# Kernel optimization log

Measured on AMD Instinct MI355X. Metric: run time of the kernel, lower is better.

The kernel has to match this reference:

```python
import jax, jax.numpy as jnp
import numpy as np

N = 200_000      # n_reflns
NIMG = 500       # n_images
DMETA = 24       # metadata features
WIDTH = 32       # mlp_width
HID = 64         # hidden_units = 2*width (FeedForward default)
DEPTH = 20       # mlp_depth
NPOST = 2        # Normal posterior: (loc, scale)
EPS = 1e-12
KLW = 0.01       # scaling_kl_weight


def setup_inputs() -> dict:
    key = jax.random.key(0)
    ks = jax.random.split(key, 10)
    metadata = jax.random.normal(ks[0], (N, DMETA), jnp.float32)
    iobs = jax.random.normal(ks[1], (N, 1), jnp.float32)
    sigiobs = jax.random.uniform(ks[2], (N, 1), jnp.float32)
    image_ids = jnp.sort(jax.random.randint(ks[3], (N,), 0, NIMG)).astype(jnp.int32)
    n_reflns_per_image = jnp.bincount(image_ids, length=NIMG).astype(jnp.int32)
    d_img = DMETA + 2  # concat(metadata, iobs, sigiobs)
    w_img_in = jax.random.normal(ks[4], (d_img, WIDTH), jnp.float32) / np.float32(np.sqrt(d_img))
    b_img_in = jnp.zeros((WIDTH,), jnp.float32)
    w_scale_in = jax.random.normal(ks[5], (DMETA, WIDTH), jnp.float32) / np.float32(np.sqrt(DMETA))
    b_scale_in = jnp.zeros((WIDTH,), jnp.float32)
    # shared residual FeedForward stack (share_weights=True): x + W2 @ relu(W1 @ x)
    mlp_w1 = jax.random.normal(ks[6], (DEPTH, WIDTH, HID), jnp.float32) / np.float32(np.sqrt(WIDTH))
    mlp_b1 = jnp.zeros((DEPTH, HID), jnp.float32)
    mlp_w2 = jax.random.normal(ks[7], (DEPTH, HID, WIDTH), jnp.float32) * np.float32(0.1 / np.sqrt(HID))
    mlp_b2 = jnp.zeros((DEPTH, WIDTH), jnp.float32)
    w_out = jax.random.normal(ks[8], (WIDTH, NPOST), jnp.float32) / np.float32(np.sqrt(WIDTH))
    b_out = jnp.zeros((NPOST,), jnp.float32)
    return {
        'metadata': metadata, 'iobs': iobs, 'sigiobs': sigiobs,
        'w_img_in': w_img_in, 'b_img_in': b_img_in,
        'w_scale_in': w_scale_in, 'b_scale_in': b_scale_in,
        'mlp_w1': mlp_w1, 'mlp_b1': mlp_b1, 'mlp_w2': mlp_w2, 'mlp_b2': mlp_b2,
        'w_out': w_out, 'b_out': b_out,
        'image_ids_in_this_batch': image_ids,
        'n_reflns_per_image': n_reflns_per_image,
        'mc_samples': 32,
    }


def _mlp(h, w1, b1, w2, b2):
    # depth residual FF blocks, weights stacked along leading DEPTH axis
    def block(h, ws):
        wa, ba, wb, bb = ws
        h = h + (jax.nn.relu(h @ wa + ba) @ wb + bb)
        return h, None
    h, _ = jax.lax.scan(block, h, (w1, b1, w2, b2))
    return h


def reference(metadata, iobs, sigiobs,
              w_img_in, b_img_in, w_scale_in, b_scale_in,
              mlp_w1, mlp_b1, mlp_w2, mlp_b2, w_out, b_out,
              image_ids_in_this_batch, n_reflns_per_image, mc_samples):
    image = jnp.concatenate([metadata, iobs, sigiobs], axis=-1)   # (N, DMETA+2)
    h = image @ w_img_in + b_img_in                               # (N, W)
    h = _mlp(h, mlp_w1, mlp_b1, mlp_w2, mlp_b2)
    nimg = n_reflns_per_image.shape[0]
    sums = jax.ops.segment_sum(h, image_ids_in_this_batch, num_segments=nimg)
    counts = jnp.maximum(n_reflns_per_image, 1).astype(h.dtype)[:, None]
    pooled = sums / counts                                        # (NIMG, W) image-average pool
    s = metadata @ w_scale_in + b_scale_in + pooled[image_ids_in_this_batch]
    s = _mlp(s, mlp_w1, mlp_b1, mlp_w2, mlp_b2)                   # shared weights
    params = s @ w_out + b_out                                    # (N, 2)
    loc = params[:, 0]
    scale = jax.nn.softplus(params[:, 1]) + EPS
    # rsample from Normal(loc, scale), mc_samples draws
    noise = jax.random.normal(jax.random.key(42), (mc_samples, loc.shape[0]), loc.dtype)
    z = loc + scale * noise                                       # (S, N)
    # MC KL estimate: mean_s[log q(z) - log p(z)], p = Laplace(0, 1)
    log_q = -0.5 * jnp.square(noise) - jnp.log(scale) - np.float32(0.5 * np.log(2.0 * np.pi))
    log_p = -jnp.abs(z) - np.float32(np.log(2.0))
    kl_div = KLW * jnp.mean(log_q - log_p, axis=0)                # (N,)
    return z.T, kl_div
```

## Files before the change

### kernel.cpp

```cpp
#include <hip/hip_runtime.h>
#include <stdint.h>

#define N_ROWS 200000
#define NIMG   500
#define DMETA  24
#define WIDTH  32
#define HID    64
#define DEPTH  20
#define MC     32


#define WB      64000
#define LSTR2   16768
#define OFF_WI  (WB + DEPTH * LSTR2)
#define OFF_WS  (OFF_WI + 4096)
#define OFF_BIQ (OFF_WS + 4096)
#define OFF_BSQ (OFF_BIQ + 128)
#define OFF_WOQ (OFF_BSQ + 128)

typedef __attribute__((ext_vector_type(8))) short bf16x8;
typedef __attribute__((ext_vector_type(4))) float f32x4;
typedef __attribute__((ext_vector_type(16))) float f32x16;

#define MFMA32(a, b, acc) __builtin_amdgcn_mfma_f32_32x32x16_bf16((a), (b), (acc), 0, 0, 0)
#define SWP(x, y) asm("v_permlane32_swap_b32 %0, %1" : "+v"(x), "+v"(y))
#define WOFFi(h5, reg) ((((reg) & 3) + 8 * ((reg) >> 2)) + 4 * (h5))

__device__ __forceinline__ uint32_t rotl32(uint32_t x, int r) {
    return (x << r) | (x >> (32 - r));
}

__device__ __forceinline__ uint32_t tf_bits(uint32_t j) {
    const uint32_t ks1 = 42u, ks2 = 0x1BD11BDAu ^ 42u;
    uint32_t x0 = 0u, x1 = j + ks1;
#define R4(a,b,c,d) \
    x0 += x1; x1 = rotl32(x1,(a)); x1 ^= x0; \
    x0 += x1; x1 = rotl32(x1,(b)); x1 ^= x0; \
    x0 += x1; x1 = rotl32(x1,(c)); x1 ^= x0; \
    x0 += x1; x1 = rotl32(x1,(d)); x1 ^= x0;
    R4(13,15,26,6)  x0 += ks1; x1 += ks2 + 1u;
    R4(17,29,16,24) x0 += ks2; x1 += 0u + 2u;
    R4(13,15,26,6)                x1 += ks1 + 3u;
    R4(17,29,16,24) x0 += ks1; x1 += ks2 + 4u;
    R4(13,15,26,6)  x0 += ks2; x1 += 0u + 5u;
#undef R4
    return x0 ^ x1;
}

__device__ __forceinline__ float bits_to_normal(uint32_t b) {
    float f = __uint_as_float((b >> 9) | 0x3f800000u) - 1.0f;
    const float lo = -0.99999994f;
    float u = fmaxf(lo, f * 2.0f + lo);
    return 1.41421356f * erfinvf(u);
}

__device__ __forceinline__ void split1(float x, short& hi, short& lo) {
    uint32_t b = __float_as_uint(x);
    uint32_t a = b + 0x8000u;
    hi = (short)(a >> 16);
    float r = x - __uint_as_float(a & 0xFFFF0000u);
    lo = (short)(__float_as_uint(r) >> 16);
}

__device__ __forceinline__ void split8p(const float* x, bf16x8& hi, bf16x8& lo) {
    uint32_t hu[4], lu[4];
#pragma unroll
    for (int p = 0; p < 4; ++p) {
        float x0 = x[2 * p], x1 = x[2 * p + 1];
        uint32_t h;
        asm("v_cvt_pk_bf16_f32 %0, %1, %2" : "=v"(h) : "v"(x0), "v"(x1));
        float r0 = x0 - __uint_as_float(h << 16);
        float r1 = x1 - __uint_as_float(h & 0xFFFF0000u);
        uint32_t l;
        asm("v_cvt_pk_bf16_f32 %0, %1, %2" : "=v"(l) : "v"(r0), "v"(r1));
        hu[p] = h;
        lu[p] = l;
    }
    __builtin_memcpy(&hi, hu, 16);
    __builtin_memcpy(&lo, lu, 16);
}

__device__ __forceinline__ void mkbfrag(const float* h, bf16x8* Bh, bf16x8* Bl) {
    uint32_t Hh[8], Hl[8];
#pragma unroll
    for (int p = 0; p < 8; ++p) {
        float x0 = h[2 * p], x1 = h[2 * p + 1];
        uint32_t wd;
        asm("v_cvt_pk_bf16_f32 %0, %1, %2" : "=v"(wd) : "v"(x0), "v"(x1));
        float r0 = x0 - __uint_as_float(wd << 16);
        float r1 = x1 - __uint_as_float(wd & 0xFFFF0000u);
        uint32_t ld;
        asm("v_cvt_pk_bf16_f32 %0, %1, %2" : "=v"(ld) : "v"(r0), "v"(r1));
        Hh[p] = wd;
        Hl[p] = ld;
    }
    SWP(Hh[0], Hh[2]); SWP(Hh[1], Hh[3]); SWP(Hh[4], Hh[6]); SWP(Hh[5], Hh[7]);
    SWP(Hl[0], Hl[2]); SWP(Hl[1], Hl[3]); SWP(Hl[4], Hl[6]); SWP(Hl[5], Hl[7]);
    __builtin_memcpy(&Bh[0], &Hh[0], 16);
    __builtin_memcpy(&Bh[1], &Hh[4], 16);
    __builtin_memcpy(&Bl[0], &Hl[0], 16);
    __builtin_memcpy(&Bl[1], &Hl[4], 16);
}

__device__ __forceinline__ void mlp20_x2(float* h0, float* h1,
                                         const char* __restrict__ wsb,
                                         int lane, int h5) {
    uint32_t lb = WB;
    const uint32_t lf = (uint32_t)(lane * 16);
#pragma unroll 1
    for (int l = 0; l < DEPTH; ++l) {
        bf16x8 B0h[2], B0l[2], B1h[2], B1l[2];
        mkbfrag(h0, B0h, B0l);
        mkbfrag(h1, B1h, B1l);
        uint32_t P0[16], P1[16];
#pragma unroll
        for (int tm = 0; tm < 2; ++tm) {
            f32x16 acc0, acc1;
            {
                const char* bq = wsb + lb + 16384u + (uint32_t)(tm * 128 + h5 * 64);
#pragma unroll
                for (int r = 0; r < 4; ++r) {
                    f32x4 q = *(const f32x4*)(bq + 16 * r);
#pragma unroll
                    for (int i = 0; i < 4; ++i) {
                        acc0[4 * r + i] = q[i];
                        acc1[4 * r + i] = q[i];
                    }
                }
            }
            const char* fa = wsb + lb + lf + (uint32_t)(tm * 4096);
            bf16x8 a0h = *(const bf16x8*)(fa);
            bf16x8 a0l = *(const bf16x8*)(fa + 1024);
            bf16x8 a1h = *(const bf16x8*)(fa + 2048);
            bf16x8 a1l = *(const bf16x8*)(fa + 3072);
            acc0 = MFMA32(a0h, B0h[0], acc0);
            acc1 = MFMA32(a0h, B1h[0], acc1);
            acc0 = MFMA32(a0h, B0l[0], acc0);
            acc1 = MFMA32(a0h, B1l[0], acc1);
            acc0 = MFMA32(a0l, B0h[0], acc0);
            acc1 = MFMA32(a0l, B1h[0], acc1);
            acc0 = MFMA32(a1h, B0h[1], acc0);
            acc1 = MFMA32(a1h, B1h[1], acc1);
            acc0 = MFMA32(a1h, B0l[1], acc0);
            acc1 = MFMA32(a1h, B1l[1], acc1);
            acc0 = MFMA32(a1l, B0h[1], acc0);
            acc1 = MFMA32(a1l, B1h[1], acc1);
#pragma unroll
            for (int p = 0; p < 8; ++p) {
                float f0 = fmaxf(acc0[2 * p], 0.0f);
                float f1 = fmaxf(acc0[2 * p + 1], 0.0f);
                uint32_t wd;
                asm("v_cvt_pk_bf16_f32 %0, %1, %2" : "=v"(wd) : "v"(f0), "v"(f1));
                P0[tm * 8 + p] = wd;
                float g0 = fmaxf(acc1[2 * p], 0.0f);
                float g1 = fmaxf(acc1[2 * p + 1], 0.0f);
                uint32_t we;
                asm("v_cvt_pk_bf16_f32 %0, %1, %2" : "=v"(we) : "v"(g0), "v"(g1));
                P1[tm * 8 + p] = we;
            }
        }
        SWP(P0[0], P0[2]);  SWP(P0[1], P0[3]);  SWP(P0[4], P0[6]);   SWP(P0[5], P0[7]);
        SWP(P0[8], P0[10]); SWP(P0[9], P0[11]); SWP(P0[12], P0[14]); SWP(P0[13], P0[15]);
        SWP(P1[0], P1[2]);  SWP(P1[1], P1[3]);  SWP(P1[4], P1[6]);   SWP(P1[5], P1[7]);
        SWP(P1[8], P1[10]); SWP(P1[9], P1[11]); SWP(P1[12], P1[14]); SWP(P1[13], P1[15]);
        f32x16 acc20, acc21;
        {
            const char* bq = wsb + lb + 16640u + (uint32_t)(h5 * 64);
#pragma unroll
            for (int r = 0; r < 4; ++r) {
                f32x4 q = *(const f32x4*)(bq + 16 * r);
#pragma unroll
                for (int i = 0; i < 4; ++i) {
                    acc20[4 * r + i] = h0[4 * r + i] + q[i];
                    acc21[4 * r + i] = h1[4 * r + i] + q[i];
                }
            }
        }
#pragma unroll
        for (int ks = 0; ks < 4; ++ks) {
            bf16x8 Bk0, Bk1;
            __builtin_memcpy(&Bk0, &P0[ks * 4], 16);
            __builtin_memcpy(&Bk1, &P1[ks * 4], 16);
            const char* fa = wsb + lb + lf + 8192u + (uint32_t)(ks * 2048);
            bf16x8 ah = *(const bf16x8*)(fa);
            bf16x8 al = *(const bf16x8*)(fa + 1024);
            acc20 = MFMA32(ah, Bk0, acc20);
            acc21 = MFMA32(ah, Bk1, acc21);
            acc20 = MFMA32(al, Bk0, acc20);
            acc21 = MFMA32(al, Bk1, acc21);
        }
#pragma unroll
        for (int i = 0; i < 16; ++i) { h0[i] = acc20[i]; h1[i] = acc21[i]; }
        lb += LSTR2;
    }
}

__device__ __forceinline__ void input_proj32_x2(
    const bf16x8* X0, const bf16x8* X1,
    const char* __restrict__ wsb, uint32_t wfoff, uint32_t bqoff,
    float* h0, float* h1, int lane, int h5) {
    f32x16 acc0, acc1;
    {
        const char* bq = wsb + bqoff + (uint32_t)(h5 * 64);
#pragma unroll
        for (int r = 0; r < 4; ++r) {
            f32x4 q = *(const f32x4*)(bq + 16 * r);
#pragma unroll
            for (int i = 0; i < 4; ++i) { acc0[4 * r + i] = q[i]; acc1[4 * r + i] = q[i]; }
        }
    }
    const char* fa = wsb + wfoff + (uint32_t)(lane * 16);
    bf16x8 a0h = *(const bf16x8*)(fa);
    bf16x8 a0l = *(const bf16x8*)(fa + 1024);
    bf16x8 a1h = *(const bf16x8*)(fa + 2048);
    bf16x8 a1l = *(const bf16x8*)(fa + 3072);
    acc0 = MFMA32(a0h, X0[0], acc0);
    acc1 = MFMA32(a0h, X1[0], acc1);
    acc0 = MFMA32(a0h, X0[1], acc0);
    acc1 = MFMA32(a0h, X1[1], acc1);
    acc0 = MFMA32(a0l, X0[0], acc0);
    acc1 = MFMA32(a0l, X1[0], acc1);
    acc0 = MFMA32(a1h, X0[2], acc0);
    acc1 = MFMA32(a1h, X1[2], acc1);
    acc0 = MFMA32(a1h, X0[3], acc0);
    acc1 = MFMA32(a1h, X1[3], acc1);
    acc0 = MFMA32(a1l, X0[2], acc0);
    acc1 = MFMA32(a1l, X1[2], acc1);
#pragma unroll
    for (int i = 0; i < 16; ++i) { h0[i] = acc0[i]; h1[i] = acc1[i]; }
}

__device__ __forceinline__ void load_xfrags(
    const float* __restrict__ md, const float* __restrict__ iobs,
    const float* __restrict__ sig, int row, int h5, bf16x8* X) {
    float xa0[8], xa1[8];
    {
        const f32x4* rp = (const f32x4*)(md + (size_t)row * DMETA + 8 * h5);
        f32x4 a = rp[0], b = rp[1];
#pragma unroll
        for (int j = 0; j < 4; ++j) { xa0[j] = a[j]; xa0[4 + j] = b[j]; }
    }
    if (h5 == 0) {
        const f32x4* rp = (const f32x4*)(md + (size_t)row * DMETA + 16);
        f32x4 a = rp[0], b = rp[1];
#pragma unroll
        for (int j = 0; j < 4; ++j) { xa1[j] = a[j]; xa1[4 + j] = b[j]; }
    } else {
        xa1[0] = iobs ? iobs[row] : 0.0f;
        xa1[1] = sig ? sig[row] : 0.0f;
#pragma unroll
        for (int j = 2; j < 8; ++j) xa1[j] = 0.0f;
    }
    split8p(xa0, X[0], X[1]);
    split8p(xa1, X[2], X[3]);
}

__global__ __launch_bounds__(256) void prep_kernel(
    const float* __restrict__ w1, const float* __restrict__ w2,
    const float* __restrict__ wimg, const float* __restrict__ wsc,
    const float* __restrict__ b1, const float* __restrict__ b2,
    const float* __restrict__ bimg, const float* __restrict__ bsc,
    const float* __restrict__ wout, char* __restrict__ wsb) {
    int t = blockIdx.x * 256 + threadIdx.x;
    float* sums = (float*)wsb;
    if (t < 16000) { sums[t] = 0.0f; return; }
    t -= 16000;
    if (t < 40960) {
        int l = t >> 11, r = t & 2047;
        int tm = r >> 10, ks = (r >> 9) & 1, lane = (r >> 3) & 63, j = r & 7;
        int k = 16 * ks + 8 * (lane >> 5) + j;
        int u = 32 * tm + (lane & 31);
        short hh, ll;
        split1(w1[l * 2048 + k * 64 + u], hh, ll);
        char* base = wsb + WB + l * LSTR2 + (tm * 2 + ks) * 2048 + 2 * (lane * 8 + j);
        *(short*)base = hh;
        *(short*)(base + 1024) = ll;
        return;
    }
    t -= 40960;
    if (t < 40960) {
        int l = t >> 11, r = t & 2047;
        int ks = r >> 9, lane = (r >> 3) & 63, j = r & 7;
        int u = 16 * ks + 8 * (lane >> 5) + j;
        int w = lane & 31;
        short hh, ll;
        split1(w2[l * 2048 + u * 32 + w], hh, ll);
        char* base = wsb + WB + l * LSTR2 + 8192 + ks * 2048 + 2 * (lane * 8 + j);
        *(short*)base = hh;
        *(short*)(base + 1024) = ll;
        return;
    }
    t -= 40960;
    if (t < 1280) {
        int l = t >> 6, r = t & 63;
        int tm = r >> 5, h5 = (r >> 4) & 1, reg = r & 15;
        *(float*)(wsb + WB + l * LSTR2 + 16384 + tm * 128 + h5 * 64 + reg * 4) =
            b1[l * 64 + 32 * tm + WOFFi(h5, reg)];
        return;
    }
    t -= 1280;
    if (t < 640) {
        int l = t >> 5, r = t & 31;
        int h5 = r >> 4, reg = r & 15;
        *(float*)(wsb + WB + l * LSTR2 + 16640 + h5 * 64 + reg * 4) =
            b2[l * 32 + WOFFi(h5, reg)];
        return;
    }
    t -= 640;
    if (t < 1024) {
        int ks = t >> 9, lane = (t >> 3) & 63, j = t & 7;
        int d = 16 * ks + 8 * (lane >> 5) + j, w = lane & 31;
        float v = (d < 26) ? wimg[d * 32 + w] : 0.0f;
        short hh, ll;
        split1(v, hh, ll);
        char* base = wsb + OFF_WI + ks * 2048 + 2 * (lane * 8 + j);
        *(short*)base = hh;
        *(short*)(base + 1024) = ll;
        return;
    }
    t -= 1024;
    if (t < 1024) {
        int ks = t >> 9, lane = (t >> 3) & 63, j = t & 7;
        int d = 16 * ks + 8 * (lane >> 5) + j, w = lane & 31;
        float v = (d < 24) ? wsc[d * 32 + w] : 0.0f;
        short hh, ll;
        split1(v, hh, ll);
        char* base = wsb + OFF_WS + ks * 2048 + 2 * (lane * 8 + j);
        *(short*)base = hh;
        *(short*)(base + 1024) = ll;
        return;
    }
    t -= 1024;
    if (t < 32) {
        int h5 = t >> 4, reg = t & 15;
        *(float*)(wsb + OFF_BIQ + h5 * 64 + reg * 4) = bimg[WOFFi(h5, reg)];
        return;
    }
    t -= 32;
    if (t < 32) {
        int h5 = t >> 4, reg = t & 15;
        *(float*)(wsb + OFF_BSQ + h5 * 64 + reg * 4) = bsc[WOFFi(h5, reg)];
        return;
    }
    t -= 32;
    if (t < 64) {
        int h5 = t >> 5, r = t & 31, reg = r >> 1, comp = r & 1;
        *(float*)(wsb + OFF_WOQ + h5 * 128 + reg * 8 + comp * 4) =
            wout[WOFFi(h5, reg) * 2 + comp];
        return;
    }
}

__global__ __launch_bounds__(128, 3) void pass_a(
    const float* __restrict__ md, const float* __restrict__ iobs,
    const float* __restrict__ sig, const char* __restrict__ wsb,
    const int* __restrict__ ids, float* __restrict__ sums) {
    int lane = threadIdx.x & 63, wv = threadIdx.x >> 6;
    int h5 = lane >> 5;
    int gw = blockIdx.x * 2 + wv;
    int R = gw * 64;
    if (R >= N_ROWS) return;
    int row0 = R + (lane & 31), row1 = row0 + 32;

    bf16x8 X0[4], X1[4];
    load_xfrags(md, iobs, sig, row0, h5, X0);
    load_xfrags(md, iobs, sig, row1, h5, X1);

    float h0[16], h1[16];
    input_proj32_x2(X0, X1, wsb, OFF_WI, OFF_BIQ, h0, h1, lane, h5);
    mlp20_x2(h0, h1, wsb, lane, h5);

#pragma unroll
    for (int tile = 0; tile < 2; ++tile) {
        float* h = tile ? h1 : h0;
        int tb = R + tile * 32;
        int rowt = tile ? row1 : row0;
        int id0 = ids[tb];
        bool uni = (id0 == ids[tb + 31]);
        if (uni) {
#pragma unroll
            for (int m = 1; m < 32; m <<= 1) {
#pragma unroll
                for (int i = 0; i < 16; ++i) h[i] += __shfl_xor(h[i], m, 64);
            }
            if ((lane & 31) == 0) {
#pragma unroll
                for (int i = 0; i < 16; ++i)
                    atomicAdd(&sums[id0 * 32 + WOFFi(h5, i)], h[i]);
            }
        } else {
            int id = ids[rowt];
#pragma unroll
            for (int i = 0; i < 16; ++i)
                atomicAdd(&sums[id * 32 + WOFFi(h5, i)], h[i]);
        }
    }
}

__global__ __launch_bounds__(256) void normalize_kernel(float* __restrict__ sums,
                                                        const int* __restrict__ cnts) {
    int t = blockIdx.x * 256 + threadIdx.x;
    if (t < NIMG * WIDTH) {
        int img = t >> 5;
        float cc = (float)max(cnts[img], 1);
        sums[t] = sums[t] / cc;
    }
}

__global__ __launch_bounds__(128, 3) void pass_b(
    const float* __restrict__ md, const char* __restrict__ wsb,
    const float* __restrict__ bout, const int* __restrict__ ids,
    const float* __restrict__ pooled, float* __restrict__ out) {
    int lane = threadIdx.x & 63, wv = threadIdx.x >> 6;
    int h5 = lane >> 5;
    int gw = blockIdx.x * 2 + wv;
    int R = gw * 64;
    if (R >= N_ROWS) return;
    int row0 = R + (lane & 31), row1 = row0 + 32;

    bf16x8 X0[4], X1[4];
    load_xfrags(md, nullptr, nullptr, row0, h5, X0);
    load_xfrags(md, nullptr, nullptr, row1, h5, X1);

    float h0[16], h1[16];
    input_proj32_x2(X0, X1, wsb, OFF_WS, OFF_BSQ, h0, h1, lane, h5);

#pragma unroll
    for (int tile = 0; tile < 2; ++tile) {
        float* h = tile ? h1 : h0;
        int idp = ids[tile ? row1 : row0];
#pragma unroll
        for (int a = 0; a < 4; ++a) {
            f32x4 q = *(const f32x4*)(pooled + idp * 32 + 8 * a + 4 * h5);
#pragma unroll
            for (int i = 0; i < 4; ++i) h[4 * a + i] += q[i];
        }
    }

    mlp20_x2(h0, h1, wsb, lane, h5);

    f32x4 wq[8];
    {
        const char* wp = wsb + OFF_WOQ + (uint32_t)(h5 * 128);
#pragma unroll
        for (int r = 0; r < 8; ++r) wq[r] = *(const f32x4*)(wp + 16 * r);
    }
#pragma unroll
    for (int tile = 0; tile < 2; ++tile) {
        const float* h = tile ? h1 : h0;
        int row = tile ? row1 : row0;
        float p0 = 0.0f, p1 = 0.0f;
#pragma unroll
        for (int r = 0; r < 8; ++r) {
            p0 = fmaf(h[2 * r], wq[r][0], p0);
            p1 = fmaf(h[2 * r], wq[r][1], p1);
            p0 = fmaf(h[2 * r + 1], wq[r][2], p0);
            p1 = fmaf(h[2 * r + 1], wq[r][3], p1);
        }
        p0 += __shfl_xor(p0, 32, 64);
        p1 += __shfl_xor(p1, 32, 64);
        float loc = p0 + bout[0];
        float pb = p1 + bout[1];
        float scale = fmaxf(pb, 0.0f) + log1pf(expf(-fabsf(pb))) + 1e-12f;
        float lsg = logf(scale);

        float kp = 0.0f;
        float* zrow = out + (size_t)row * MC + h5 * 16;
#pragma unroll 4
        for (int s4 = 0; s4 < 4; ++s4) {
            f32x4 zv;
#pragma unroll
            for (int jj = 0; jj < 4; ++jj) {
                int tt = h5 * 16 + s4 * 4 + jj;
                uint32_t j = (uint32_t)(tt * N_ROWS) + (uint32_t)row;
                float n = bits_to_normal(tf_bits(j));
                float z = fmaf(scale, n, loc);
                zv[jj] = z;
                kp += fmaf(-0.5f, n * n, fabsf(z));
            }
            *(f32x4*)(zrow + s4 * 4) = zv;
        }
        kp += __shfl_xor(kp, 32, 64);
        if (h5 == 0) {
            out[(size_t)N_ROWS * MC + row] =
                0.01f * (kp * (1.0f / 32.0f) - lsg - 0.91893853320467274f + 0.69314718055994531f);
        }
    }
}

extern "C" void kernel_launch(void* const* d_in, const int* in_sizes, int n_in,
                              void* d_out, int out_size, void* d_ws, size_t ws_size,
                              hipStream_t stream) {
    const float* md   = (const float*)d_in[0];
    const float* iobs = (const float*)d_in[1];
    const float* sig  = (const float*)d_in[2];
    const float* wimg = (const float*)d_in[3];
    const float* bimg = (const float*)d_in[4];
    const float* wsc  = (const float*)d_in[5];
    const float* bsc  = (const float*)d_in[6];
    const float* w1   = (const float*)d_in[7];
    const float* b1   = (const float*)d_in[8];
    const float* w2   = (const float*)d_in[9];
    const float* b2   = (const float*)d_in[10];
    const float* wout = (const float*)d_in[11];
    const float* bout = (const float*)d_in[12];
    const int* ids    = (const int*)d_in[13];
    const int* cnts   = (const int*)d_in[14];
    float* out = (float*)d_out;
    char* wsb = (char*)d_ws;
    float* sums = (float*)wsb;

    const int nblk = 1563;
    prep_kernel<<<399, 256, 0, stream>>>(w1, w2, wimg, wsc, b1, b2, bimg, bsc, wout, wsb);
    pass_a<<<nblk, 128, 0, stream>>>(md, iobs, sig, wsb, ids, sums);
    normalize_kernel<<<(NIMG * WIDTH + 255) / 256, 256, 0, stream>>>(sums, cnts);
    pass_b<<<nblk, 128, 0, stream>>>(md, wsb, bout, ids, sums, out);
}
```

Measured before the change: 391.5 us.

## Stage MLP weights in double-buffered LDS with per-layer prefetch

Before, both MLP passes read each layer's bf16 weight fragments and biases straight from global memory. They now copy the fragments into a double-buffered shared-memory tile, loading the next layer into registers while the current layer computes. All biases are preloaded into shared memory once. Blocks grow to 256 threads (4 waves) so a block shares each staged layer, with a __syncthreads per layer and inactive tail waves kept alive for the barriers. In exchange this adds barrier stalls, about 40KB of LDS per block that may limit occupancy, and extra register pressure from the staging buffers.

```diff
diff --git a/kernel.cpp b/kernel.cpp
--- a/kernel.cpp
+++ b/kernel.cpp
@@ -102,13 +102,23 @@
     __builtin_memcpy(&Bl[1], &Hl[4], 16);
 }
 
-__device__ __forceinline__ void mlp20_x2(float* h0, float* h1,
-                                         const char* __restrict__ wsb,
-                                         int lane, int h5) {
-    uint32_t lb = WB;
+__device__ __forceinline__ void mlp20_x2(
+    float* h0, float* h1, char* lfr0, const char* lbias,
+    const char* __restrict__ wsb, int wv, int lane, int h5) {
     const uint32_t lf = (uint32_t)(lane * 16);
+    const uint32_t sc = (uint32_t)(wv * 4096) + lf;
+    uint32_t boff = 0;
+    int cur = 0;
 #pragma unroll 1
     for (int l = 0; l < DEPTH; ++l) {
+        f32x4 stg[4];
+        if (l < DEPTH - 1) {
+            const char* srcn = wsb + WB + (l + 1) * LSTR2;
+#pragma unroll
+            for (int i = 0; i < 4; ++i)
+                stg[i] = *(const f32x4*)(srcn + sc + (uint32_t)(i * 1024));
+        }
+        const char* cb = lfr0 + cur * 16384;
         bf16x8 B0h[2], B0l[2], B1h[2], B1l[2];
         mkbfrag(h0, B0h, B0l);
         mkbfrag(h1, B1h, B1l);
@@ -117,7 +127,7 @@
         for (int tm = 0; tm < 2; ++tm) {
             f32x16 acc0, acc1;
             {
-                const char* bq = wsb + lb + 16384u + (uint32_t)(tm * 128 + h5 * 64);
+                const char* bq = lbias + boff + (uint32_t)(tm * 128 + h5 * 64);
 #pragma unroll
                 for (int r = 0; r < 4; ++r) {
                     f32x4 q = *(const f32x4*)(bq + 16 * r);
@@ -128,7 +138,7 @@
                     }
                 }
             }
-            const char* fa = wsb + lb + lf + (uint32_t)(tm * 4096);
+            const char* fa = cb + (uint32_t)(tm * 4096) + lf;
             bf16x8 a0h = *(const bf16x8*)(fa);
             bf16x8 a0l = *(const bf16x8*)(fa + 1024);
             bf16x8 a1h = *(const bf16x8*)(fa + 2048);
@@ -165,7 +175,7 @@
         SWP(P1[8], P1[10]); SWP(P1[9], P1[11]); SWP(P1[12], P1[14]); SWP(P1[13], P1[15]);
         f32x16 acc20, acc21;
         {
-            const char* bq = wsb + lb + 16640u + (uint32_t)(h5 * 64);
+            const char* bq = lbias + boff + 256u + (uint32_t)(h5 * 64);
 #pragma unroll
             for (int r = 0; r < 4; ++r) {
                 f32x4 q = *(const f32x4*)(bq + 16 * r);
@@ -181,7 +191,7 @@
             bf16x8 Bk0, Bk1;
             __builtin_memcpy(&Bk0, &P0[ks * 4], 16);
             __builtin_memcpy(&Bk1, &P1[ks * 4], 16);
-            const char* fa = wsb + lb + lf + 8192u + (uint32_t)(ks * 2048);
+            const char* fa = cb + 8192u + (uint32_t)(ks * 2048) + lf;
             bf16x8 ah = *(const bf16x8*)(fa);
             bf16x8 al = *(const bf16x8*)(fa + 1024);
             acc20 = MFMA32(ah, Bk0, acc20);
@@ -191,7 +201,15 @@
         }
 #pragma unroll
         for (int i = 0; i < 16; ++i) { h0[i] = acc20[i]; h1[i] = acc21[i]; }
-        lb += LSTR2;
+        if (l < DEPTH - 1) {
+            char* db = lfr0 + (cur ^ 1) * 16384;
+#pragma unroll
+            for (int i = 0; i < 4; ++i)
+                *(f32x4*)(db + sc + (uint32_t)(i * 1024)) = stg[i];
+        }
+        __syncthreads();
+        cur ^= 1;
+        boff += 384;
     }
 }
 
@@ -351,16 +369,28 @@
     }
 }
 
-__global__ __launch_bounds__(128, 3) void pass_a(
+__global__ __launch_bounds__(256, 4) void pass_a(
     const float* __restrict__ md, const float* __restrict__ iobs,
     const float* __restrict__ sig, const char* __restrict__ wsb,
     const int* __restrict__ ids, float* __restrict__ sums) {
+    __shared__ __attribute__((aligned(16))) char lfr[2][16384];
+    __shared__ __attribute__((aligned(16))) char lbias[7680];
     int lane = threadIdx.x & 63, wv = threadIdx.x >> 6;
     int h5 = lane >> 5;
-    int gw = blockIdx.x * 2 + wv;
-    int R = gw * 64;
-    if (R >= N_ROWS) return;
-    int row0 = R + (lane & 31), row1 = row0 + 32;
+    int R = blockIdx.x * 256 + wv * 64;
+    bool act = (R < N_ROWS);
+    int Rb = act ? R : 0;
+    int row0 = Rb + (lane & 31), row1 = row0 + 32;
+
+    f32x4 stg[4];
+    const uint32_t sc = (uint32_t)(wv * 4096 + lane * 16);
+#pragma unroll
+    for (int i = 0; i < 4; ++i)
+        stg[i] = *(const f32x4*)(wsb + WB + sc + (uint32_t)(i * 1024));
+    for (int c = threadIdx.x; c < 480; c += 256) {
+        int l = c / 24, o = (c % 24) * 16;
+        *(f32x4*)(lbias + c * 16) = *(const f32x4*)(wsb + WB + l * LSTR2 + 16384 + o);
+    }
 
     bf16x8 X0[4], X1[4];
     load_xfrags(md, iobs, sig, row0, h5, X0);
@@ -368,8 +398,15 @@
 
     float h0[16], h1[16];
     input_proj32_x2(X0, X1, wsb, OFF_WI, OFF_BIQ, h0, h1, lane, h5);
-    mlp20_x2(h0, h1, wsb, lane, h5);
-
+
+#pragma unroll
+    for (int i = 0; i < 4; ++i)
+        *(f32x4*)(&lfr[0][0] + sc + (uint32_t)(i * 1024)) = stg[i];
+    __syncthreads();
+
+    mlp20_x2(h0, h1, &lfr[0][0], lbias, wsb, wv, lane, h5);
+
+    if (!act) return;
 #pragma unroll
     for (int tile = 0; tile < 2; ++tile) {
         float* h = tile ? h1 : h0;
@@ -407,16 +444,28 @@
     }
 }
 
-__global__ __launch_bounds__(128, 3) void pass_b(
+__global__ __launch_bounds__(256, 4) void pass_b(
     const float* __restrict__ md, const char* __restrict__ wsb,
     const float* __restrict__ bout, const int* __restrict__ ids,
     const float* __restrict__ pooled, float* __restrict__ out) {
+    __shared__ __attribute__((aligned(16))) char lfr[2][16384];
+    __shared__ __attribute__((aligned(16))) char lbias[7680];
     int lane = threadIdx.x & 63, wv = threadIdx.x >> 6;
     int h5 = lane >> 5;
-    int gw = blockIdx.x * 2 + wv;
-    int R = gw * 64;
-    if (R >= N_ROWS) return;
-    int row0 = R + (lane & 31), row1 = row0 + 32;
+    int R = blockIdx.x * 256 + wv * 64;
+    bool act = (R < N_ROWS);
+    int Rb = act ? R : 0;
+    int row0 = Rb + (lane & 31), row1 = row0 + 32;
+
+    f32x4 stg[4];
+    const uint32_t sc = (uint32_t)(wv * 4096 + lane * 16);
+#pragma unroll
+    for (int i = 0; i < 4; ++i)
+        stg[i] = *(const f32x4*)(wsb + WB + sc + (uint32_t)(i * 1024));
+    for (int c = threadIdx.x; c < 480; c += 256) {
+        int l = c / 24, o = (c % 24) * 16;
+        *(f32x4*)(lbias + c * 16) = *(const f32x4*)(wsb + WB + l * LSTR2 + 16384 + o);
+    }
 
     bf16x8 X0[4], X1[4];
     load_xfrags(md, nullptr, nullptr, row0, h5, X0);
@@ -437,8 +486,14 @@
         }
     }
 
-    mlp20_x2(h0, h1, wsb, lane, h5);
-
+#pragma unroll
+    for (int i = 0; i < 4; ++i)
+        *(f32x4*)(&lfr[0][0] + sc + (uint32_t)(i * 1024)) = stg[i];
+    __syncthreads();
+
+    mlp20_x2(h0, h1, &lfr[0][0], lbias, wsb, wv, lane, h5);
+
+    if (!act) return;
     f32x4 wq[8];
     {
         const char* wp = wsb + OFF_WOQ + (uint32_t)(h5 * 128);
@@ -510,9 +565,9 @@
     char* wsb = (char*)d_ws;
     float* sums = (float*)wsb;
 
-    const int nblk = 1563;
+    const int nblk = 782;
     prep_kernel<<<399, 256, 0, stream>>>(w1, w2, wimg, wsc, b1, b2, bimg, bsc, wout, wsb);
-    pass_a<<<nblk, 128, 0, stream>>>(md, iobs, sig, wsb, ids, sums);
+    pass_a<<<nblk, 256, 0, stream>>>(md, iobs, sig, wsb, ids, sums);
     normalize_kernel<<<(NIMG * WIDTH + 255) / 256, 256, 0, stream>>>(sums, cnts);
-    pass_b<<<nblk, 128, 0, stream>>>(md, wsb, bout, ids, sums, out);
-}
+    pass_b<<<nblk, 256, 0, stream>>>(md, wsb, bout, ids, sums, out);
+}
```

Result: slower. 413.9 us (+5.7%).
